# Optimization experiments

Hardware: AMD Instinct MI355X
Metric: run time of the kernel (lower is better)

Reference implementation:

```python
import math
import jax, jax.numpy as jnp
import numpy as np

B, T, D, L, E = 2, 1024, 1024, 12, 4
EPS = 1e-5


def _ln(v, g, b):
    mu = jnp.mean(v, axis=-1, keepdims=True)
    var = jnp.mean(jnp.square(v - mu), axis=-1, keepdims=True)
    return (v - mu) * jax.lax.rsqrt(var + EPS) * g + b


def setup_inputs() -> dict:
    key = jax.random.key(0)
    ks = jax.random.split(key, 4)
    x = jax.random.normal(ks[0], (B, T, D), dtype=jnp.float32)
    queries = jax.random.normal(ks[1], (L, D), dtype=jnp.float32) * 0.02
    W1 = jax.random.normal(ks[2], (L, D, E * D), dtype=jnp.float32) * 0.02
    W2 = jax.random.normal(ks[3], (L, E * D, D), dtype=jnp.float32) * 0.02
    return {
        'x': x,
        'queries': queries,
        'kn_g': jnp.ones((L, D), jnp.float32),
        'kn_b': jnp.zeros((L, D), jnp.float32),
        'ln_g': jnp.ones((L, D), jnp.float32),
        'ln_b': jnp.zeros((L, D), jnp.float32),
        'W1': W1,
        'b1': jnp.zeros((L, E * D), jnp.float32),
        'W2': W2,
        'b2': jnp.zeros((L, D), jnp.float32),
    }


def reference(x, queries, kn_g, kn_b, ln_g, ln_b, W1, b1, W2, b2):
    scale = 1.0 / math.sqrt(D)
    history = [x]
    h = x
    for l in range(L):
        V = jnp.stack(history, axis=0)              # (l+1, B, T, D)
        K = _ln(V, kn_g[l], kn_b[l])
        scores = jnp.einsum('d,lbtd->lbt', queries[l], K) * scale
        alpha = jax.nn.softmax(scores, axis=0)       # softmax over history axis
        residual = jnp.einsum('lbt,lbtd->btd', alpha, V)
        u = _ln(h, ln_g[l], ln_b[l])
        ff = jax.nn.gelu(u @ W1[l] + b1[l], approximate=False) @ W2[l] + b2[l]
        h = residual + ff
        history.append(h)
    return h
```

## Files before the change

### kernel.cpp

```cpp
#include <hip/hip_runtime.h>
#include <math.h>

#define BATCH 2
#define TSEQ 1024
#define DIM 1024
#define NLAYER 12
#define EDIM 4096
#define BT 2048
#define EPS_LN 1e-5f
#define NZ2 2

typedef __attribute__((ext_vector_type(4))) float  f32x4;
typedef __attribute__((ext_vector_type(8))) __bf16 bf16x8;
typedef __attribute__((ext_vector_type(4))) __bf16 bf16x4;

__device__ __forceinline__ void gl_lds16(const void* gptr, void* lptr) {
    __builtin_amdgcn_global_load_lds(
        (const __attribute__((address_space(1))) void*)gptr,
        (__attribute__((address_space(3))) void*)lptr,
        16, 0, 0);
}

__device__ __forceinline__ void wtile256(float (*t)[65], const float* src,
                                         __bf16* dst, int R, int C,
                                         int rt, int ct, int tid)
{
    int lr = tid >> 2, cs = (tid & 3) << 4;
    const float* sp = src + (size_t)(rt * 64 + lr) * C + ct * 64 + cs;
#pragma unroll
    for (int s = 0; s < 4; s++) {
        f32x4 v = *(const f32x4*)(sp + s * 4);
        t[lr][cs + s * 4 + 0] = v[0];
        t[lr][cs + s * 4 + 1] = v[1];
        t[lr][cs + s * 4 + 2] = v[2];
        t[lr][cs + s * 4 + 3] = v[3];
    }
    __syncthreads();
    int oc = tid >> 2, rs = (tid & 3) << 4;
    bf16x8 o0, o1;
#pragma unroll
    for (int e = 0; e < 8; e++) o0[e] = (__bf16)t[rs + e][oc];
#pragma unroll
    for (int e = 0; e < 8; e++) o1[e] = (__bf16)t[rs + 8 + e][oc];
    __bf16* dp = dst + (size_t)(ct * 64 + oc) * R + rt * 64 + rs;
    *(bf16x8*)dp = o0;
    *(bf16x8*)(dp + 8) = o1;
}

__global__ __launch_bounds__(256) void wtrans_kernel(
    const float* __restrict__ W1, const float* __restrict__ W2,
    __bf16* __restrict__ W1t, __bf16* __restrict__ W2t)
{
    __shared__ float t[64][65];
    int z = blockIdx.z;
    if (z == 0) wtile256(t, W1, W1t, DIM, EDIM, blockIdx.y, blockIdx.x, threadIdx.x);
    else        wtile256(t, W2, W2t, EDIM, DIM, blockIdx.x, blockIdx.y, threadIdx.x);
}

__global__ __launch_bounds__(256)
void attn_wt_kernel(const float* __restrict__ x,
                    const float* __restrict__ baseprev,
                    __bf16* __restrict__ histbf,
                    const __bf16* __restrict__ part,
                    const float* __restrict__ q,
                    const float* __restrict__ kng,
                    const float* __restrict__ knb,
                    const float* __restrict__ lng,
                    const float* __restrict__ lnb,
                    const float* __restrict__ b2,
                    float* __restrict__ hnext,
                    __bf16* __restrict__ u,
                    int nl,
                    const float* __restrict__ W1n,
                    const float* __restrict__ W2n,
                    __bf16* __restrict__ W1tn,
                    __bf16* __restrict__ W2tn,
                    int dowt)
{
    __shared__ char smem[49408];

    if (blockIdx.x >= BT) {
        if (!dowt) return;
        float (*t)[65] = (float(*)[65])smem;
        int tile = blockIdx.x - BT;
        if (tile < 1024) wtile256(t, W1n, W1tn, DIM, EDIM, tile >> 6, tile & 63, threadIdx.x);
        else { int t3 = tile - 1024; wtile256(t, W2n, W2tn, EDIM, DIM, t3 & 63, t3 >> 6, threadIdx.x); }
        return;
    }

    float (*V)[DIM] = (float(*)[DIM])smem;
    float* sS  = (float*)(smem + 49152);
    float* sMu = sS + NLAYER;
    float* sRs = sMu + NLAYER;

    const int bt = blockIdx.x;
    const int tid = threadIdx.x, lane = tid & 63, w = tid >> 6;

    f32x4 gqv[4];
    float sg = 0.f, sb = 0.f;
#pragma unroll
    for (int i = 0; i < 4; i++) {
        int d = i * 256 + lane * 4;
        f32x4 g4 = *(const f32x4*)(kng + d);
        f32x4 q4 = *(const f32x4*)(q + d);
        f32x4 b4 = *(const f32x4*)(knb + d);
#pragma unroll
        for (int c = 0; c < 4; c++) {
            float gq = g4[c] * q4[c];
            gqv[i][c] = gq;
            sg += gq;
            sb += b4[c] * q4[c];
        }
    }
#pragma unroll
    for (int off = 32; off; off >>= 1) {
        sg += __shfl_xor(sg, off);
        sb += __shfl_xor(sb, off);
    }

    for (int lp = w; lp < nl; lp += 4) {
        f32x4 vv[4];
        if (lp == nl - 1) {
            const float* vp = (nl == 1) ? (x + (size_t)bt * DIM)
                                        : (baseprev + (size_t)bt * DIM);
#pragma unroll
            for (int i = 0; i < 4; i++) vv[i] = *(const f32x4*)(vp + i * 256 + lane * 4);
            if (part) {
#pragma unroll
                for (int z = 0; z < NZ2; z++) {
                    const __bf16* pp = part + ((size_t)z * BT + bt) * DIM;
#pragma unroll
                    for (int i = 0; i < 4; i++) {
                        bf16x4 p4 = *(const bf16x4*)(pp + i * 256 + lane * 4);
#pragma unroll
                        for (int c = 0; c < 4; c++) vv[i][c] += (float)p4[c];
                    }
                }
            }
            if (nl < NLAYER) {
                __bf16* mp = histbf + ((size_t)lp * BT + bt) * DIM;
#pragma unroll
                for (int i = 0; i < 4; i++) {
                    bf16x4 m4;
#pragma unroll
                    for (int c = 0; c < 4; c++) m4[c] = (__bf16)vv[i][c];
                    *(bf16x4*)(mp + i * 256 + lane * 4) = m4;
                }
            }
        } else {
            const __bf16* mp = histbf + ((size_t)lp * BT + bt) * DIM;
#pragma unroll
            for (int i = 0; i < 4; i++) {
                bf16x4 m4 = *(const bf16x4*)(mp + i * 256 + lane * 4);
#pragma unroll
                for (int c = 0; c < 4; c++) vv[i][c] = (float)m4[c];
            }
        }

        float s1 = 0.f, s2 = 0.f, sq = 0.f;
#pragma unroll
        for (int i = 0; i < 4; i++) {
            *(f32x4*)(&V[lp][i * 256 + lane * 4]) = vv[i];
#pragma unroll
            for (int c = 0; c < 4; c++) {
                float xv = vv[i][c];
                s1 += xv; s2 += xv * xv; sq += xv * gqv[i][c];
            }
        }
#pragma unroll
        for (int off = 32; off; off >>= 1) {
            s1 += __shfl_xor(s1, off);
            s2 += __shfl_xor(s2, off);
            sq += __shfl_xor(sq, off);
        }
        if (lane == 0) {
            float mu = s1 * (1.0f / DIM);
            float var = s2 * (1.0f / DIM) - mu * mu;
            float rs = rsqrtf(var + EPS_LN);
            sMu[lp] = mu; sRs[lp] = rs;
            sS[lp] = (rs * (sq - mu * sg) + sb) * (1.0f / 32.0f);
        }
    }
    __syncthreads();

    float mx = -1e30f;
#pragma unroll
    for (int i = 0; i < NLAYER; i++) if (i < nl) mx = fmaxf(mx, sS[i]);
    float al[NLAYER];
    float ssum = 0.f;
#pragma unroll
    for (int i = 0; i < NLAYER; i++) {
        al[i] = (i < nl) ? __expf(sS[i] - mx) : 0.f;
        ssum += al[i];
    }
    float inv = 1.0f / ssum;

    const int d = tid * 4;
    f32x4 r; r[0] = 0.f; r[1] = 0.f; r[2] = 0.f; r[3] = 0.f;
#pragma unroll
    for (int i = 0; i < NLAYER; i++) {
        if (i < nl) {
            f32x4 v4 = *(const f32x4*)(&V[i][d]);
            float a = al[i] * inv;
            r[0] += a * v4[0]; r[1] += a * v4[1]; r[2] += a * v4[2]; r[3] += a * v4[3];
        }
    }
    f32x4 h4 = *(const f32x4*)(&V[nl - 1][d]);
    f32x4 b24 = *(const f32x4*)(b2 + d);
    f32x4 ro; ro[0] = r[0] + b24[0]; ro[1] = r[1] + b24[1];
    ro[2] = r[2] + b24[2]; ro[3] = r[3] + b24[3];
    *(f32x4*)(hnext + (size_t)bt * DIM + d) = ro;

    float mu = sMu[nl - 1], rs = sRs[nl - 1];
    f32x4 g4 = *(const f32x4*)(lng + d);
    f32x4 b4 = *(const f32x4*)(lnb + d);
    bf16x4 uo;
#pragma unroll
    for (int c = 0; c < 4; c++) uo[c] = (__bf16)((h4[c] - mu) * rs * g4[c] + b4[c]);
    *(bf16x4*)(u + (size_t)bt * DIM + d) = uo;
}

#define STG 49152

template <int EPI, int NT>
__global__ __launch_bounds__(512, 1)
void gemm8(const __bf16* __restrict__ A, const __bf16* __restrict__ Bt,
           const float* __restrict__ bias, void* __restrict__ outp,
           int N, int As, int Bs)
{
    __shared__ char lds[3 * STG];
    const int tid = threadIdx.x, lane = tid & 63, w = tid >> 6;
    const int wm = w >> 2, wn = w & 3;
    const int lr = lane & 15;
    const int hib = (lane >> 4) << 4;

    const int fid = blockIdx.x;
    const int m0 = (fid & 15) * 128;
    const int n0 = (fid >> 4) * 256;
    const int kbase = blockIdx.y * (NT * 64);

    f32x4 acc[4][4];
#pragma unroll
    for (int i = 0; i < 4; i++)
#pragma unroll
        for (int j = 0; j < 4; j++) { acc[i][j][0]=0.f; acc[i][j][1]=0.f; acc[i][j][2]=0.f; acc[i][j][3]=0.f; }

    const int srow = tid >> 3;
    const int ksrc = ((tid & 7) << 4) ^ ((srow & 7) << 4);
    const char* Ac = (const char*)A;
    const char* Bc = (const char*)Bt;
    size_t aoff[2], boff[4];
#pragma unroll
    for (int c = 0; c < 2; c++)
        aoff[c] = ((size_t)(m0 + c * 64 + srow) * As + kbase) * 2 + ksrc;
#pragma unroll
    for (int c = 0; c < 4; c++)
        boff[c] = ((size_t)(n0 + c * 64 + srow) * Bs + kbase) * 2 + ksrc;

    char* abw = lds + w * 1024;
    char* bbw = lds + 16384 + w * 1024;

    auto STAGE = [&](int tt, int bi) {
        size_t kb = (size_t)tt * 128;
        char* ab = abw + bi * STG;
        char* bb = bbw + bi * STG;
#pragma unroll
        for (int c = 0; c < 2; c++) gl_lds16(Ac + aoff[c] + kb, ab + c * 8192);
#pragma unroll
        for (int c = 0; c < 4; c++) gl_lds16(Bc + boff[c] + kb, bb + c * 8192);
    };

    STAGE(0, 0);
    STAGE(1, 1);

    int sb = 0, st = 2;
#pragma unroll 1
    for (int t = 0; t < NT; ++t) {
        if (t < NT - 1) asm volatile("s_waitcnt vmcnt(6)" ::: "memory");
        else            asm volatile("s_waitcnt vmcnt(0)" ::: "memory");
        __builtin_amdgcn_s_barrier();
        __builtin_amdgcn_sched_barrier(0);

        if (t + 2 < NT) STAGE(t + 2, st);

        const char* base = lds + sb * STG;
        bf16x8 af[2][4], bfr[2][4];
#pragma unroll
        for (int kk = 0; kk < 2; kk++) {
#pragma unroll
            for (int i = 0; i < 4; i++) {
                int ra = wm * 64 + i * 16 + lr;
                af[kk][i] = *(const bf16x8*)(base + ra * 128 + ((kk * 64 + hib) ^ ((ra & 7) << 4)));
            }
#pragma unroll
            for (int j = 0; j < 4; j++) {
                int rb = wn * 64 + j * 16 + lr;
                bfr[kk][j] = *(const bf16x8*)(base + 16384 + rb * 128 + ((kk * 64 + hib) ^ ((rb & 7) << 4)));
            }
        }
        __builtin_amdgcn_s_setprio(1);
#pragma unroll
        for (int kk = 0; kk < 2; kk++)
#pragma unroll
            for (int i = 0; i < 4; i++)
#pragma unroll
                for (int j = 0; j < 4; j++)
                    acc[i][j] = __builtin_amdgcn_mfma_f32_16x16x32_bf16(af[kk][i], bfr[kk][j], acc[i][j], 0, 0, 0);
        __builtin_amdgcn_s_setprio(0);

        sb = (sb == 2) ? 0 : sb + 1;
        st = (st == 2) ? 0 : st + 1;
    }

    const int lrow = (lane >> 4) << 2;
    if (EPI == 0) {
        __bf16* out = (__bf16*)outp;
#pragma unroll
        for (int i = 0; i < 4; i++) {
#pragma unroll
            for (int j = 0; j < 4; j++) {
                int colg = n0 + wn * 64 + j * 16 + lr;
                float bc = bias[colg];
#pragma unroll
                for (int r = 0; r < 4; r++) {
                    int rowg = m0 + wm * 64 + i * 16 + lrow + r;
                    float v = acc[i][j][r] + bc;
                    float tt2 = 0.7978845608f * (v + 0.044715f * v * v * v);
                    float e = __expf(2.0f * tt2);
                    float th = 1.0f - 2.0f / (e + 1.0f);
                    out[(size_t)rowg * N + colg] = (__bf16)(0.5f * v * (1.0f + th));
                }
            }
        }
    } else {
        __bf16* out = (__bf16*)outp + (size_t)blockIdx.y * BT * N;
#pragma unroll
        for (int i = 0; i < 4; i++) {
#pragma unroll
            for (int j = 0; j < 4; j++) {
                int colg = n0 + wn * 64 + j * 16 + lr;
#pragma unroll
                for (int r = 0; r < 4; r++) {
                    int rowg = m0 + wm * 64 + i * 16 + lrow + r;
                    out[(size_t)rowg * N + colg] = (__bf16)acc[i][j][r];
                }
            }
        }
    }
}

__global__ void final_reduce(const float* __restrict__ base,
                             const __bf16* __restrict__ part,
                             float* __restrict__ out)
{
    size_t i = ((size_t)blockIdx.x * 256 + threadIdx.x) * 4;
    f32x4 r = *(const f32x4*)(base + i);
#pragma unroll
    for (int z = 0; z < NZ2; z++) {
        bf16x4 p = *(const bf16x4*)(part + (size_t)z * BT * DIM + i);
#pragma unroll
        for (int c = 0; c < 4; c++) r[c] += (float)p[c];
    }
    *(f32x4*)(out + i) = r;
}

extern "C" void kernel_launch(void* const* d_in, const int* in_sizes, int n_in,
                              void* d_out, int out_size, void* d_ws, size_t ws_size,
                              hipStream_t stream)
{
    const float* x   = (const float*)d_in[0];
    const float* q   = (const float*)d_in[1];
    const float* kng = (const float*)d_in[2];
    const float* knb = (const float*)d_in[3];
    const float* lng = (const float*)d_in[4];
    const float* lnb = (const float*)d_in[5];
    const float* W1  = (const float*)d_in[6];
    const float* b1  = (const float*)d_in[7];
    const float* W2  = (const float*)d_in[8];
    const float* b2  = (const float*)d_in[9];

    char* ws = (char*)d_ws;
    const size_t MB = 1048576;
    float*  base2[2] = { (float*)(ws), (float*)(ws + 8 * MB) };
    __bf16* histbf = (__bf16*)(ws + 16 * MB);
    __bf16* ubuf   = (__bf16*)(ws + 64 * MB);
    __bf16* hmid   = (__bf16*)(ws + 68 * MB);
    __bf16* W1tb[2] = { (__bf16*)(ws + 84 * MB), (__bf16*)(ws + 92 * MB) };
    __bf16* W2tb[2] = { (__bf16*)(ws + 100 * MB), (__bf16*)(ws + 108 * MB) };
    __bf16* part   = (__bf16*)(ws + 116 * MB);

    wtrans_kernel<<<dim3(64, 16, 2), 256, 0, stream>>>(W1, W2, W1tb[0], W2tb[0]);

    for (int l = 0; l < NLAYER; l++) {
        int nl = l + 1;
        int ln = (l + 1 < NLAYER) ? l + 1 : l;
        float* hnext = base2[l & 1];
        const float* bprev = base2[(l + 1) & 1];
        attn_wt_kernel<<<dim3(2 * BT), 256, 0, stream>>>(
            x, bprev, histbf, (l >= 1) ? part : (const __bf16*)nullptr,
            q + (size_t)l * DIM,
            kng + (size_t)l * DIM, knb + (size_t)l * DIM,
            lng + (size_t)l * DIM, lnb + (size_t)l * DIM,
            b2 + (size_t)l * DIM, hnext, ubuf, nl,
            W1 + (size_t)ln * DIM * EDIM, W2 + (size_t)ln * EDIM * DIM,
            W1tb[(l + 1) & 1], W2tb[(l + 1) & 1], (l + 1 < NLAYER) ? 1 : 0);
        gemm8<0, 16><<<dim3(256, 1), 512, 0, stream>>>(
            ubuf, W1tb[l & 1], b1 + (size_t)l * EDIM, (void*)hmid, EDIM, DIM, DIM);
        gemm8<2, 32><<<dim3(64, NZ2), 512, 0, stream>>>(
            hmid, W2tb[l & 1], nullptr, (void*)part, DIM, EDIM, EDIM);
    }

    final_reduce<<<dim3(BT * DIM / 1024), 256, 0, stream>>>(
        base2[1], part, (float*)d_out);
}
```

Before: 979.6 us.

## Store residual base in bf16, raise W2 split-K to 4, swizzle GEMM tile order

The residual base buffer (attention output plus b2) is now stored in bf16 instead of fp32, which halves its read and write traffic in the attention and final-reduce kernels. The second GEMM's split-K factor goes from 2 to 4 with half the K-tiles per block, giving 256 blocks instead of 128 so more CUs are busy. The cost is more partial-sum traffic for the next layer to reduce. GEMM blocks are remapped into 8x4 groups of tiles so neighbouring blocks share A and B tiles in cache. Storing the residual in bf16 adds rounding error that accumulates over layers.

```diff
diff --git a/kernel.cpp b/kernel.cpp
--- a/kernel.cpp
+++ b/kernel.cpp
@@ -8,7 +8,7 @@
 #define EDIM 4096
 #define BT 2048
 #define EPS_LN 1e-5f
-#define NZ2 2
+#define NZ2 4
 
 typedef __attribute__((ext_vector_type(4))) float  f32x4;
 typedef __attribute__((ext_vector_type(8))) __bf16 bf16x8;
@@ -59,7 +59,7 @@
 
 __global__ __launch_bounds__(256)
 void attn_wt_kernel(const float* __restrict__ x,
-                    const float* __restrict__ baseprev,
+                    const __bf16* __restrict__ baseprev,
                     __bf16* __restrict__ histbf,
                     const __bf16* __restrict__ part,
                     const float* __restrict__ q,
@@ -68,7 +68,7 @@
                     const float* __restrict__ lng,
                     const float* __restrict__ lnb,
                     const float* __restrict__ b2,
-                    float* __restrict__ hnext,
+                    __bf16* __restrict__ hnext,
                     __bf16* __restrict__ u,
                     int nl,
                     const float* __restrict__ W1n,
@@ -121,10 +121,19 @@
     for (int lp = w; lp < nl; lp += 4) {
         f32x4 vv[4];
         if (lp == nl - 1) {
-            const float* vp = (nl == 1) ? (x + (size_t)bt * DIM)
-                                        : (baseprev + (size_t)bt * DIM);
-#pragma unroll
-            for (int i = 0; i < 4; i++) vv[i] = *(const f32x4*)(vp + i * 256 + lane * 4);
+            if (nl == 1) {
+                const float* vp = x + (size_t)bt * DIM;
+#pragma unroll
+                for (int i = 0; i < 4; i++) vv[i] = *(const f32x4*)(vp + i * 256 + lane * 4);
+            } else {
+                const __bf16* vp = baseprev + (size_t)bt * DIM;
+#pragma unroll
+                for (int i = 0; i < 4; i++) {
+                    bf16x4 b4 = *(const bf16x4*)(vp + i * 256 + lane * 4);
+#pragma unroll
+                    for (int c = 0; c < 4; c++) vv[i][c] = (float)b4[c];
+                }
+            }
             if (part) {
 #pragma unroll
                 for (int z = 0; z < NZ2; z++) {
@@ -207,9 +216,10 @@
     }
     f32x4 h4 = *(const f32x4*)(&V[nl - 1][d]);
     f32x4 b24 = *(const f32x4*)(b2 + d);
-    f32x4 ro; ro[0] = r[0] + b24[0]; ro[1] = r[1] + b24[1];
-    ro[2] = r[2] + b24[2]; ro[3] = r[3] + b24[3];
-    *(f32x4*)(hnext + (size_t)bt * DIM + d) = ro;
+    bf16x4 ho;
+#pragma unroll
+    for (int c = 0; c < 4; c++) ho[c] = (__bf16)(r[c] + b24[c]);
+    *(bf16x4*)(hnext + (size_t)bt * DIM + d) = ho;
 
     float mu = sMu[nl - 1], rs = sRs[nl - 1];
     f32x4 g4 = *(const f32x4*)(lng + d);
@@ -235,15 +245,18 @@
     const int hib = (lane >> 4) << 4;
 
     const int fid = blockIdx.x;
-    const int m0 = (fid & 15) * 128;
-    const int n0 = (fid >> 4) * 256;
+    const int g = fid >> 5, j = fid & 31;
+    const int mi = (j & 7) + ((g & 1) << 3);
+    const int ni = (j >> 3) + ((g >> 1) << 2);
+    const int m0 = mi * 128;
+    const int n0 = ni * 256;
     const int kbase = blockIdx.y * (NT * 64);
 
     f32x4 acc[4][4];
 #pragma unroll
     for (int i = 0; i < 4; i++)
 #pragma unroll
-        for (int j = 0; j < 4; j++) { acc[i][j][0]=0.f; acc[i][j][1]=0.f; acc[i][j][2]=0.f; acc[i][j][3]=0.f; }
+        for (int j2 = 0; j2 < 4; j2++) { acc[i][j2][0]=0.f; acc[i][j2][1]=0.f; acc[i][j2][2]=0.f; acc[i][j2][3]=0.f; }
 
     const int srow = tid >> 3;
     const int ksrc = ((tid & 7) << 4) ^ ((srow & 7) << 4);
@@ -293,9 +306,9 @@
                 af[kk][i] = *(const bf16x8*)(base + ra * 128 + ((kk * 64 + hib) ^ ((ra & 7) << 4)));
             }
 #pragma unroll
-            for (int j = 0; j < 4; j++) {
-                int rb = wn * 64 + j * 16 + lr;
-                bfr[kk][j] = *(const bf16x8*)(base + 16384 + rb * 128 + ((kk * 64 + hib) ^ ((rb & 7) << 4)));
+            for (int j2 = 0; j2 < 4; j2++) {
+                int rb = wn * 64 + j2 * 16 + lr;
+                bfr[kk][j2] = *(const bf16x8*)(base + 16384 + rb * 128 + ((kk * 64 + hib) ^ ((rb & 7) << 4)));
             }
         }
         __builtin_amdgcn_s_setprio(1);
@@ -304,8 +317,8 @@
 #pragma unroll
             for (int i = 0; i < 4; i++)
 #pragma unroll
-                for (int j = 0; j < 4; j++)
-                    acc[i][j] = __builtin_amdgcn_mfma_f32_16x16x32_bf16(af[kk][i], bfr[kk][j], acc[i][j], 0, 0, 0);
+                for (int j2 = 0; j2 < 4; j2++)
+                    acc[i][j2] = __builtin_amdgcn_mfma_f32_16x16x32_bf16(af[kk][i], bfr[kk][j2], acc[i][j2], 0, 0, 0);
         __builtin_amdgcn_s_setprio(0);
 
         sb = (sb == 2) ? 0 : sb + 1;
@@ -318,13 +331,13 @@
 #pragma unroll
         for (int i = 0; i < 4; i++) {
 #pragma unroll
-            for (int j = 0; j < 4; j++) {
-                int colg = n0 + wn * 64 + j * 16 + lr;
+            for (int j2 = 0; j2 < 4; j2++) {
+                int colg = n0 + wn * 64 + j2 * 16 + lr;
                 float bc = bias[colg];
 #pragma unroll
                 for (int r = 0; r < 4; r++) {
                     int rowg = m0 + wm * 64 + i * 16 + lrow + r;
-                    float v = acc[i][j][r] + bc;
+                    float v = acc[i][j2][r] + bc;
                     float tt2 = 0.7978845608f * (v + 0.044715f * v * v * v);
                     float e = __expf(2.0f * tt2);
                     float th = 1.0f - 2.0f / (e + 1.0f);
@@ -337,24 +350,27 @@
 #pragma unroll
         for (int i = 0; i < 4; i++) {
 #pragma unroll
-            for (int j = 0; j < 4; j++) {
-                int colg = n0 + wn * 64 + j * 16 + lr;
+            for (int j2 = 0; j2 < 4; j2++) {
+                int colg = n0 + wn * 64 + j2 * 16 + lr;
 #pragma unroll
                 for (int r = 0; r < 4; r++) {
                     int rowg = m0 + wm * 64 + i * 16 + lrow + r;
-                    out[(size_t)rowg * N + colg] = (__bf16)acc[i][j][r];
+                    out[(size_t)rowg * N + colg] = (__bf16)acc[i][j2][r];
                 }
             }
         }
     }
 }
 
-__global__ void final_reduce(const float* __restrict__ base,
+__global__ void final_reduce(const __bf16* __restrict__ base,
                              const __bf16* __restrict__ part,
                              float* __restrict__ out)
 {
     size_t i = ((size_t)blockIdx.x * 256 + threadIdx.x) * 4;
-    f32x4 r = *(const f32x4*)(base + i);
+    bf16x4 b4 = *(const bf16x4*)(base + i);
+    f32x4 r;
+#pragma unroll
+    for (int c = 0; c < 4; c++) r[c] = (float)b4[c];
 #pragma unroll
     for (int z = 0; z < NZ2; z++) {
         bf16x4 p = *(const bf16x4*)(part + (size_t)z * BT * DIM + i);
@@ -381,21 +397,21 @@
 
     char* ws = (char*)d_ws;
     const size_t MB = 1048576;
-    float*  base2[2] = { (float*)(ws), (float*)(ws + 8 * MB) };
-    __bf16* histbf = (__bf16*)(ws + 16 * MB);
-    __bf16* ubuf   = (__bf16*)(ws + 64 * MB);
-    __bf16* hmid   = (__bf16*)(ws + 68 * MB);
-    __bf16* W1tb[2] = { (__bf16*)(ws + 84 * MB), (__bf16*)(ws + 92 * MB) };
-    __bf16* W2tb[2] = { (__bf16*)(ws + 100 * MB), (__bf16*)(ws + 108 * MB) };
-    __bf16* part   = (__bf16*)(ws + 116 * MB);
+    __bf16* base2[2] = { (__bf16*)(ws), (__bf16*)(ws + 4 * MB) };
+    __bf16* histbf = (__bf16*)(ws + 8 * MB);
+    __bf16* ubuf   = (__bf16*)(ws + 56 * MB);
+    __bf16* hmid   = (__bf16*)(ws + 60 * MB);
+    __bf16* W1tb[2] = { (__bf16*)(ws + 76 * MB), (__bf16*)(ws + 84 * MB) };
+    __bf16* W2tb[2] = { (__bf16*)(ws + 92 * MB), (__bf16*)(ws + 100 * MB) };
+    __bf16* part   = (__bf16*)(ws + 108 * MB);
 
     wtrans_kernel<<<dim3(64, 16, 2), 256, 0, stream>>>(W1, W2, W1tb[0], W2tb[0]);
 
     for (int l = 0; l < NLAYER; l++) {
         int nl = l + 1;
         int ln = (l + 1 < NLAYER) ? l + 1 : l;
-        float* hnext = base2[l & 1];
-        const float* bprev = base2[(l + 1) & 1];
+        __bf16* hnext = base2[l & 1];
+        const __bf16* bprev = base2[(l + 1) & 1];
         attn_wt_kernel<<<dim3(2 * BT), 256, 0, stream>>>(
             x, bprev, histbf, (l >= 1) ? part : (const __bf16*)nullptr,
             q + (size_t)l * DIM,
@@ -406,7 +422,7 @@
             W1tb[(l + 1) & 1], W2tb[(l + 1) & 1], (l + 1 < NLAYER) ? 1 : 0);
         gemm8<0, 16><<<dim3(256, 1), 512, 0, stream>>>(
             ubuf, W1tb[l & 1], b1 + (size_t)l * EDIM, (void*)hmid, EDIM, DIM, DIM);
-        gemm8<2, 32><<<dim3(64, NZ2), 512, 0, stream>>>(
+        gemm8<2, 16><<<dim3(64, NZ2), 512, 0, stream>>>(
             hmid, W2tb[l & 1], nullptr, (void*)part, DIM, EDIM, EDIM);
     }
 
```

After: 886.2 us. 1.11x faster.
